# Optimization experiments

Hardware: AMD Instinct MI355X
Metric: run time of the kernel (lower is better)

The kernel has to match this reference:

```python
import jax, jax.numpy as jnp
import numpy as np

V, E, H = 2048, 256, 256
B, T, MMAX = 256, 16, 96  # blocks, max tokens/instr, max instrs/block


def setup_inputs() -> dict:
    key = jax.random.key(0)
    ks = jax.random.split(key, 13)
    # instruction lengths sorted descending (enforce_sorted=True), 96 down to 33
    instr_lens = (96 - (np.arange(B) * 64) // B).astype(np.int64)
    boundaries = np.concatenate([[0], np.cumsum(instr_lens)]).astype(np.int64)
    N = int(boundaries[-1])  # total instructions = 16512
    padded_tokens = jax.random.randint(ks[0], (N, T), 1, V)
    token_lengths = jax.random.randint(ks[1], (N,), 1, T + 1)
    tmask = jnp.arange(T)[None, :] < token_lengths[:, None]
    padded_tokens = jnp.where(tmask, padded_tokens, 0)  # pad with padding_idx=0
    s = 1.0 / np.sqrt(H)
    def u(k, shape):
        return jax.random.uniform(k, shape, jnp.float32, -s, s)
    emb = u(ks[2], (V, E)).at[0].set(0.0)  # padding_idx row is zero
    return dict(
        padded_tokens=padded_tokens.astype(jnp.int64),
        token_lengths=token_lengths.astype(jnp.int64),
        instruction_lengths=jnp.asarray(instr_lens),
        instr_boundaries=jnp.asarray(boundaries),
        embedding=emb,
        w_ih_tok=u(ks[3], (4 * H, E)), w_hh_tok=u(ks[4], (4 * H, H)),
        b_ih_tok=u(ks[5], (4 * H,)), b_hh_tok=u(ks[6], (4 * H,)),
        w_ih_ins=u(ks[7], (4 * H, H)), w_hh_ins=u(ks[8], (4 * H, H)),
        b_ih_ins=u(ks[9], (4 * H,)), b_hh_ins=u(ks[10], (4 * H,)),
        w_lin=u(ks[11], (1, H)), b_lin=u(ks[12], (1,)),
    )


def _lstm_final(x, lengths, w_ih, w_hh, b_ih, b_hh):
    # x: [N, S, D] padded; returns hidden state at last valid step per sequence [N, H]
    N, S, _ = x.shape
    Hh = w_hh.shape[1]
    mask = jnp.arange(S)[:, None] < lengths[None, :]  # [S, N]
    bias = b_ih + b_hh

    def step(carry, inp):
        h, c = carry
        x_t, m = inp  # x_t: [N, D], m: [N]
        g = x_t @ w_ih.T + h @ w_hh.T + bias  # [N, 4H], PyTorch gate order i,f,g,o
        i, f, gg, o = jnp.split(g, 4, axis=-1)
        c_new = jax.nn.sigmoid(f) * c + jax.nn.sigmoid(i) * jnp.tanh(gg)
        h_new = jax.nn.sigmoid(o) * jnp.tanh(c_new)
        m = m[:, None]
        return (jnp.where(m, h_new, h), jnp.where(m, c_new, c)), None

    h0 = jnp.zeros((N, Hh), x.dtype)
    (h, _), _ = jax.lax.scan(step, (h0, h0), (jnp.swapaxes(x, 0, 1), mask))
    return h


def reference(padded_tokens, token_lengths, instruction_lengths, instr_boundaries,
              embedding, w_ih_tok, w_hh_tok, b_ih_tok, b_hh_tok,
              w_ih_ins, w_hh_ins, b_ih_ins, b_hh_ins, w_lin, b_lin):
    # token-level LSTM over all instructions (packed == masked scan)
    emb_tokens = embedding[padded_tokens]  # [N, T, E]
    instr_inputs = _lstm_final(emb_tokens, token_lengths,
                               w_ih_tok, w_hh_tok, b_ih_tok, b_hh_tok)  # [N, H]
    N = instr_inputs.shape[0]
    # regroup instructions into blocks via boundaries (pad_sequence equivalent)
    idx = instr_boundaries[:-1, None] + jnp.arange(MMAX)[None, :]  # [B, MMAX]
    valid = jnp.arange(MMAX)[None, :] < instruction_lengths[:, None]
    gathered = jnp.where(valid[..., None],
                         instr_inputs[jnp.clip(idx, 0, N - 1)], 0.0)  # [B, MMAX, H]
    final = _lstm_final(gathered, instruction_lengths,
                        w_ih_ins, w_hh_ins, b_ih_ins, b_hh_ins)  # [B, H]
    return (final @ w_lin.T + b_lin).squeeze(-1)  # [B]
```

## Files before the change

kernel.cpp:

```cpp
#include <hip/hip_runtime.h>
#include <hip/hip_bf16.h>
#include <math.h>

#define VSZ 2048
#define EDIM 256
#define HDIM 256
#define G4 1024
#define TMAX 16
#define IB 16

typedef _Float16 f16x2 __attribute__((ext_vector_type(2)));
typedef _Float16 f16x4 __attribute__((ext_vector_type(4)));
typedef _Float16 f16x8 __attribute__((ext_vector_type(8)));
typedef float f32x4 __attribute__((ext_vector_type(4)));

#define HA_STRIDE 264
#define GW_STRIDE 260

__device__ __forceinline__ float fexp2(float x) {
#if defined(__has_builtin) && __has_builtin(__builtin_amdgcn_exp2f)
  return __builtin_amdgcn_exp2f(x);
#else
  return exp2f(x);
#endif
}
__device__ __forceinline__ float frcp(float x) {
#if defined(__has_builtin) && __has_builtin(__builtin_amdgcn_rcpf)
  return __builtin_amdgcn_rcpf(x);
#else
  return 1.0f / x;
#endif
}
__device__ __forceinline__ float sigm(float x) {
  return frcp(1.0f + fexp2(x * -1.44269504f));
}
__device__ __forceinline__ float tanh_fast(float x) {
  float t = fexp2(fminf(x, 15.0f) * 2.88539008f);
  return (t - 1.0f) * frcp(t + 1.0f);
}

__device__ __forceinline__ float fdot2(f16x2 a, f16x2 b, float c) {
#if defined(__has_builtin) && __has_builtin(__builtin_amdgcn_fdot2)
  return __builtin_amdgcn_fdot2(a, b, c, false);
#else
  return c + (float)a.x * (float)b.x + (float)a.y * (float)b.y;
#endif
}

__device__ __forceinline__ float dot8h(uint4 w, float4 hv, float acc) {
  f16x2 h0 = __builtin_bit_cast(f16x2, hv.x);
  f16x2 h1 = __builtin_bit_cast(f16x2, hv.y);
  f16x2 h2 = __builtin_bit_cast(f16x2, hv.z);
  f16x2 h3 = __builtin_bit_cast(f16x2, hv.w);
  f16x2 w0 = __builtin_bit_cast(f16x2, w.x);
  f16x2 w1 = __builtin_bit_cast(f16x2, w.y);
  f16x2 w2 = __builtin_bit_cast(f16x2, w.z);
  f16x2 w3 = __builtin_bit_cast(f16x2, w.w);
  return fdot2(h3, w3, fdot2(h2, w2, fdot2(h1, w1, fdot2(h0, w0, acc))));
}

__device__ __forceinline__ bool is_f32(const void* w) {
  const unsigned short* p = (const unsigned short*)w;
  int pl = 0;
#pragma unroll
  for (int i = 0; i < 64; ++i) {
    unsigned e = (p[2 * i] >> 7) & 0xFF;
    pl += (e >= 113 && e <= 122) ? 1 : 0;
  }
  return pl < 48;
}

template <bool F32>
__device__ __forceinline__ float ldf(const void* p, long j) {
  if (F32) return ((const float*)p)[j];
  return __uint_as_float(((unsigned)((const unsigned short*)p)[j]) << 16);
}
__device__ __forceinline__ float ldf_rt(const void* p, long j, bool f32) {
  if (f32) return ((const float*)p)[j];
  return __uint_as_float(((unsigned)((const unsigned short*)p)[j]) << 16);
}
template <bool I64>
__device__ __forceinline__ int ldi(const int* p, int j) {
  return I64 ? p[2 * j] : p[j];
}
__device__ __forceinline__ int ldi_rt(const int* p, int j, bool i64) {
  return i64 ? p[2 * j] : p[j];
}

__global__ __launch_bounds__(256) void k_transp(const void* src, float* __restrict__ dst,
                                                const void* fprobe) {
  __shared__ float tile[32][33];
  __shared__ int sf;
  if (threadIdx.x == 0) sf = is_f32(fprobe) ? 1 : 0;
  __syncthreads();
  const bool f32 = (sf != 0);
  const int tx = threadIdx.x & 31, ty = threadIdx.x >> 5;
  const int r0 = blockIdx.x * 32, c0 = blockIdx.y * 32;
#pragma unroll
  for (int q = 0; q < 4; ++q) {
    int rr = ty + q * 8;
    tile[rr][tx] = ldf_rt(src, (long)(r0 + rr) * 256 + (c0 + tx), f32);
  }
  __syncthreads();
#pragma unroll
  for (int q = 0; q < 4; ++q) {
    int cc = ty + q * 8;
    dst[(size_t)(c0 + cc) * 1024 + (r0 + tx)] = tile[tx][cc];
  }
}

__global__ __launch_bounds__(256) void k_pack(const void* src, uint4* __restrict__ dst,
                                              const void* fprobe) {
  __shared__ int sf;
  if (threadIdx.x == 0) sf = is_f32(fprobe) ? 1 : 0;
  __syncthreads();
  const bool f32 = (sf != 0);
  const int idx = blockIdx.x * 256 + threadIdx.x;
  const int rr = idx & 255, j = (idx >> 8) & 3, c = idx >> 10;
  const long base = (long)(j * 256 + rr) * 256 + 8 * c;
  unsigned u[4];
#pragma unroll
  for (int q = 0; q < 4; ++q) {
    f16x2 v;
    v.x = (_Float16)ldf_rt(src, base + 2 * q, f32);
    v.y = (_Float16)ldf_rt(src, base + 2 * q + 1, f32);
    u[q] = __builtin_bit_cast(unsigned, v);
  }
  uint4 o; o.x = u[0]; o.y = u[1]; o.z = u[2]; o.w = u[3];
  dst[idx] = o;
}

__global__ __launch_bounds__(256) void k_packB(const void* src, f16x8* __restrict__ dst,
                                               const void* fprobe) {
  __shared__ int sf;
  if (threadIdx.x == 0) sf = is_f32(fprobe) ? 1 : 0;
  __syncthreads();
  const bool f32 = (sf != 0);
  const int idx = blockIdx.x * 256 + threadIdx.x;
  const int l = idx & 63;
  int rest = idx >> 6;
  const int kt = rest & 7; rest >>= 3;
  const int nt = rest & 15;
  const int w = rest >> 4;
  const int n = 256 * w + nt * 16 + (l & 15);
  const int j = n & 3, e = n >> 2;
  const long base = (long)(j * 256 + e) * 256 + kt * 32 + ((l >> 4) << 3);
  f16x8 v;
#pragma unroll
  for (int q = 0; q < 8; ++q) v[q] = (_Float16)ldf_rt(src, base + q, f32);
  dst[idx] = v;
}

template <bool F32>
__device__ void tok_table_impl(const void* emb, const float* __restrict__ wT,
                               const void* bih, const void* bhh,
                               f16x4* __restrict__ tabi4, float (*xs)[256]) {
  const int t = threadIdx.x;
  const int v0 = blockIdx.x * 16;
#pragma unroll
  for (int i = 0; i < 16; ++i) xs[i][t] = ldf<F32>(emb, (long)(v0 + i) * EDIM + t);
  __syncthreads();
  float acc[4][16];
#pragma unroll
  for (int j = 0; j < 4; ++j)
#pragma unroll
    for (int i = 0; i < 16; ++i) acc[j][i] = 0.f;
  for (int k4 = 0; k4 < 64; ++k4) {
    float w[4][4];
#pragma unroll
    for (int kk = 0; kk < 4; ++kk)
#pragma unroll
      for (int j = 0; j < 4; ++j)
        w[j][kk] = wT[(size_t)(k4 * 4 + kk) * 1024 + j * 256 + t];
#pragma unroll
    for (int i = 0; i < 16; ++i) {
      float4 h4 = *(const float4*)&xs[i][k4 * 4];
#pragma unroll
      for (int j = 0; j < 4; ++j)
        acc[j][i] = fmaf(h4.x, w[j][0], fmaf(h4.y, w[j][1],
                    fmaf(h4.z, w[j][2], fmaf(h4.w, w[j][3], acc[j][i]))));
    }
  }
  float b[4];
#pragma unroll
  for (int j = 0; j < 4; ++j)
    b[j] = ldf<F32>(bih, j * 256 + t) + ldf<F32>(bhh, j * 256 + t);
#pragma unroll
  for (int i = 0; i < 16; ++i) {
    f16x4 v;
    v.x = (_Float16)(acc[0][i] + b[0]);
    v.y = (_Float16)(acc[1][i] + b[1]);
    v.z = (_Float16)(acc[2][i] + b[2]);
    v.w = (_Float16)(acc[3][i] + b[3]);
    tabi4[(size_t)(v0 + i) * 256 + t] = v;
  }
}

__global__ __launch_bounds__(256) void k_tok_table(
    const void* emb, const float* __restrict__ wT, const void* bih,
    const void* bhh, f16x4* __restrict__ tabi4, const void* fprobe) {
  __shared__ float xs[16][256];
  __shared__ int sf;
  if (threadIdx.x == 0) sf = is_f32(fprobe) ? 1 : 0;
  __syncthreads();
  if (sf) tok_table_impl<true>(emb, wT, bih, bhh, tabi4, xs);
  else    tok_table_impl<false>(emb, wT, bih, bhh, tabi4, xs);
}

__global__ __launch_bounds__(1024) void k_bucket(const int* tlen, int N,
                                                 int* __restrict__ perm,
                                                 const int* iprobe) {
  __shared__ int cnt[16][18];
  __shared__ int wbase[16][18];
  __shared__ int base[18];
  const int t = threadIdx.x;
  const int w = t >> 6;
  const bool i64 = (iprobe[1] == 0);
  if (t < 16 * 18) ((int*)cnt)[t] = 0;
  __syncthreads();
  for (int n = t; n < N; n += 1024) {
    int len = ldi_rt(tlen, n, i64);
    len = max(0, min(16, len));
    atomicAdd(&cnt[w][len], 1);
  }
  __syncthreads();
  if (t < 17) {
    int s = 0;
    for (int ww = 0; ww < 16; ++ww) { wbase[ww][t] = s; s += cnt[ww][t]; }
    base[t] = s;
  }
  __syncthreads();
  if (t == 0) {
    int s = 0;
    for (int i = 0; i <= 16; ++i) { int c = base[i]; base[i] = s; s += c; }
  }
  __syncthreads();
  if (t < 16 * 18) ((int*)cnt)[t] = 0;
  __syncthreads();
  for (int n = t; n < N; n += 1024) {
    int len = ldi_rt(tlen, n, i64);
    len = max(0, min(16, len));
    int pos = base[len] + wbase[w][len] + atomicAdd(&cnt[w][len], 1);
    perm[pos] = n;
  }
}

struct TokSmemM {
  float gateW[4][16 * GW_STRIDE];
  _Float16 hA[16 * HA_STRIDE];
  int tokL[IB][TMAX];
  int lenL[IB];
  int nIdx[IB];
};

template <bool I64>
__device__ void tok_mfma_impl(const int* tok32, const int* tlen32,
                              const int* __restrict__ perm,
                              const f16x4* __restrict__ tabi4,
                              const f16x8* __restrict__ pkB,
                              const f16x8* __restrict__ pkBI,
                              const void* bihI, const void* bhhI,
                              float* __restrict__ instrH, float* __restrict__ gx,
                              int N, int do_gx, bool f32, TokSmemM& sm) {
  const int n0 = blockIdx.x * IB, t = threadIdx.x;
  const int w = t >> 6, l = t & 63;
  if (t < IB) {
    int slot = n0 + t;
    int n = (slot < N) ? perm[slot] : -1;
    sm.nIdx[t] = n;
    sm.lenL[t] = (n >= 0) ? ldi<I64>(tlen32, n) : 0;
  }
  for (int idx = t; idx < 16 * HA_STRIDE / 2; idx += 256) ((unsigned*)sm.hA)[idx] = 0;
  __syncthreads();
  {
    int i = t >> 4, s = t & 15;
    int n = sm.nIdx[i];
    sm.tokL[i][s] = (n >= 0) ? ldi<I64>(tok32, n * TMAX + s) : 0;
  }
  float c[IB];
#pragma unroll
  for (int i = 0; i < IB; ++i) c[i] = 0.f;
  __syncthreads();
  int maxlen = 0;
#pragma unroll
  for (int i = 0; i < IB; ++i) maxlen = max(maxlen, sm.lenL[i]);

  const f16x8* Bp = pkB + (size_t)w * (16 * 8 * 64);
  const int aOff = (l & 15) * HA_STRIDE + ((l >> 4) << 3);
  const int m0 = (l >> 4) << 2;
  float* gw = sm.gateW[w];

  for (int s = 0; s < maxlen; ++s) {
    f16x8 aF[8];
#pragma unroll
    for (int kt = 0; kt < 8; ++kt)
      aF[kt] = *(const f16x8*)&sm.hA[aOff + kt * 32];
#pragma unroll 2
    for (int g4 = 0; g4 < 4; ++g4) {
      f32x4 a0 = {0.f, 0.f, 0.f, 0.f}, a1 = a0, a2 = a0, a3 = a0;
#pragma unroll
      for (int kt = 0; kt < 8; ++kt) {
        const f16x8* bb = Bp + ((size_t)(g4 * 4) * 8 + kt) * 64 + l;
        f16x8 b0 = bb[0 * 8 * 64];
        f16x8 b1 = bb[1 * 8 * 64];
        f16x8 b2 = bb[2 * 8 * 64];
        f16x8 b3 = bb[3 * 8 * 64];
        a0 = __builtin_amdgcn_mfma_f32_16x16x32_f16(aF[kt], b0, a0, 0, 0, 0);
        a1 = __builtin_amdgcn_mfma_f32_16x16x32_f16(aF[kt], b1, a1, 0, 0, 0);
        a2 = __builtin_amdgcn_mfma_f32_16x16x32_f16(aF[kt], b2, a2, 0, 0, 0);
        a3 = __builtin_amdgcn_mfma_f32_16x16x32_f16(aF[kt], b3, a3, 0, 0, 0);
      }
      const int colb = (l & 15);
#pragma unroll
      for (int r = 0; r < 4; ++r) {
        gw[(m0 + r) * GW_STRIDE + (g4 * 4 + 0) * 16 + colb] = a0[r];
        gw[(m0 + r) * GW_STRIDE + (g4 * 4 + 1) * 16 + colb] = a1[r];
        gw[(m0 + r) * GW_STRIDE + (g4 * 4 + 2) * 16 + colb] = a2[r];
        gw[(m0 + r) * GW_STRIDE + (g4 * 4 + 3) * 16 + colb] = a3[r];
      }
    }
    __syncthreads();
#pragma unroll
    for (int m = 0; m < IB; ++m) {
      if (s < sm.lenL[m]) {
        float4 gv = *(const float4*)&gw[m * GW_STRIDE + 4 * l];
        f16x4 tb = tabi4[(size_t)sm.tokL[m][s] * 256 + t];
        float gi = gv.x + (float)tb.x;
        float gf = gv.y + (float)tb.y;
        float gg = gv.z + (float)tb.z;
        float go = gv.w + (float)tb.w;
        float si = sigm(gi), sf = sigm(gf), tg = tanh_fast(gg), so = sigm(go);
        c[m] = sf * c[m] + si * tg;
        sm.hA[m * HA_STRIDE + t] = (_Float16)(so * tanh_fast(c[m]));
      }
    }
    __syncthreads();
  }
#pragma unroll
  for (int m = 0; m < IB; ++m) {
    int n = sm.nIdx[m];
    if (n >= 0) instrH[(size_t)n * HDIM + t] = (float)sm.hA[m * HA_STRIDE + t];
  }
  if (do_gx) {
    f16x8 aF[8];
#pragma unroll
    for (int kt = 0; kt < 8; ++kt)
      aF[kt] = *(const f16x8*)&sm.hA[aOff + kt * 32];
    const f16x8* BpI = pkBI + (size_t)w * (16 * 8 * 64);
#pragma unroll 2
    for (int g4 = 0; g4 < 4; ++g4) {
      f32x4 a0 = {0.f, 0.f, 0.f, 0.f}, a1 = a0, a2 = a0, a3 = a0;
#pragma unroll
      for (int kt = 0; kt < 8; ++kt) {
        const f16x8* bb = BpI + ((size_t)(g4 * 4) * 8 + kt) * 64 + l;
        f16x8 b0 = bb[0 * 8 * 64];
        f16x8 b1 = bb[1 * 8 * 64];
        f16x8 b2 = bb[2 * 8 * 64];
        f16x8 b3 = bb[3 * 8 * 64];
        a0 = __builtin_amdgcn_mfma_f32_16x16x32_f16(aF[kt], b0, a0, 0, 0, 0);
        a1 = __builtin_amdgcn_mfma_f32_16x16x32_f16(aF[kt], b1, a1, 0, 0, 0);
        a2 = __builtin_amdgcn_mfma_f32_16x16x32_f16(aF[kt], b2, a2, 0, 0, 0);
        a3 = __builtin_amdgcn_mfma_f32_16x16x32_f16(aF[kt], b3, a3, 0, 0, 0);
      }
      const int colb = (l & 15);
#pragma unroll
      for (int r = 0; r < 4; ++r) {
        gw[(m0 + r) * GW_STRIDE + (g4 * 4 + 0) * 16 + colb] = a0[r];
        gw[(m0 + r) * GW_STRIDE + (g4 * 4 + 1) * 16 + colb] = a1[r];
        gw[(m0 + r) * GW_STRIDE + (g4 * 4 + 2) * 16 + colb] = a2[r];
        gw[(m0 + r) * GW_STRIDE + (g4 * 4 + 3) * 16 + colb] = a3[r];
      }
    }
    __syncthreads();
    const float bj0 = ldf_rt(bihI, 0 * 256 + t, f32) + ldf_rt(bhhI, 0 * 256 + t, f32);
    const float bj1 = ldf_rt(bihI, 1 * 256 + t, f32) + ldf_rt(bhhI, 1 * 256 + t, f32);
    const float bj2 = ldf_rt(bihI, 2 * 256 + t, f32) + ldf_rt(bhhI, 2 * 256 + t, f32);
    const float bj3 = ldf_rt(bihI, 3 * 256 + t, f32) + ldf_rt(bhhI, 3 * 256 + t, f32);
#pragma unroll
    for (int m = 0; m < IB; ++m) {
      int n = sm.nIdx[m];
      if (n >= 0) {
        float4 gv = *(const float4*)&gw[m * GW_STRIDE + 4 * l];
        gx[(size_t)n * G4 +       t] = gv.x + bj0;
        gx[(size_t)n * G4 + 256 + t] = gv.y + bj1;
        gx[(size_t)n * G4 + 512 + t] = gv.z + bj2;
        gx[(size_t)n * G4 + 768 + t] = gv.w + bj3;
      }
    }
  }
}

__global__ __launch_bounds__(256, 2) void k_tok_lstm(
    const int* tok32, const int* tlen32, const int* __restrict__ perm,
    const f16x4* __restrict__ tabi4, const f16x8* __restrict__ pkB,
    const f16x8* __restrict__ pkBI, const void* bihI, const void* bhhI,
    float* __restrict__ instrH, float* __restrict__ gx, int N, int do_gx,
    const int* iprobe, const void* fprobe) {
  __shared__ TokSmemM sm;
  __shared__ int sfl;
  if (threadIdx.x == 0)
    sfl = ((iprobe[1] == 0) ? 1 : 0) | (is_f32(fprobe) ? 2 : 0);
  __syncthreads();
  const bool f32 = (sfl & 2) != 0;
  if (sfl & 1) tok_mfma_impl<true >(tok32, tlen32, perm, tabi4, pkB, pkBI, bihI, bhhI, instrH, gx, N, do_gx, f32, sm);
  else         tok_mfma_impl<false>(tok32, tlen32, perm, tabi4, pkB, pkBI, bihI, bhhI, instrH, gx, N, do_gx, f32, sm);
}

#define RCH 24
#define LCH 8
struct InsSmem {
  uint4 wL[LCH][1024];
  float gL[1024];
  f16x2 hL2[128];
  float red[256];
};

template <bool F32, bool I64>
__device__ void ins_rec_impl(const int* ilen32, const int* bnd32,
                             const float* __restrict__ gx,
                             const uint4* __restrict__ pk,
                             const void* wlin, const void* blin,
                             float* __restrict__ out, int B, InsSmem& sm) {
  const int b = blockIdx.x, t = threadIdx.x;
  const int j = t >> 8, rr = t & 255;
  const int len = ldi<I64>(ilen32, b);
  const long n0 = (long)ldi<I64>(bnd32, b);
#pragma unroll
  for (int cc = 0; cc < LCH; ++cc)
    sm.wL[cc][t] = pk[((RCH + cc) * 4 + j) * 256 + rr];
  uint4 wr[RCH];
#pragma unroll
  for (int cg = 0; cg < RCH; ++cg)
    wr[cg] = pk[(cg * 4 + j) * 256 + rr];
  if (t < 128) {
    f16x2 z; z.x = (_Float16)0.f; z.y = (_Float16)0.f;
    sm.hL2[t] = z;
  }
  float c = 0.f, h = 0.f;
  __syncthreads();

  for (int m = 0; m < len; ++m) {
    float g0 = 0.f, g1 = 0.f, g2 = 0.f, g3 = 0.f;
    if (t < 256) {
      const float* gp = gx + (size_t)(n0 + m) * G4;
      g0 = gp[t]; g1 = gp[256 + t]; g2 = gp[512 + t]; g3 = gp[768 + t];
    }
    float a0 = 0.f, a1 = 0.f;
#pragma unroll
    for (int cg = 0; cg < RCH; ++cg) {
      float4 hv = ((const float4*)sm.hL2)[cg];
      if (cg & 1) a1 = dot8h(wr[cg], hv, a1);
      else        a0 = dot8h(wr[cg], hv, a0);
    }
#pragma unroll
    for (int cc = 0; cc < LCH; ++cc) {
      float4 hv = ((const float4*)sm.hL2)[RCH + cc];
      if (cc & 1) a1 = dot8h(sm.wL[cc][t], hv, a1);
      else        a0 = dot8h(sm.wL[cc][t], hv, a0);
    }
    sm.gL[t] = a0 + a1;
    __syncthreads();
    if (t < 256) {
      float gi = g0 + sm.gL[t];
      float gf = g1 + sm.gL[256 + t];
      float gg = g2 + sm.gL[512 + t];
      float go = g3 + sm.gL[768 + t];
      float si = sigm(gi), sf = sigm(gf), tg = tanh_fast(gg), so = sigm(go);
      c = sf * c + si * tg;
      h = so * tanh_fast(c);
      ((_Float16*)sm.hL2)[t] = (_Float16)h;
    }
    __syncthreads();
  }
  if (t < 256) sm.red[t] = h * ldf<F32>(wlin, t);
  __syncthreads();
  for (int st = 128; st > 0; st >>= 1) {
    if (t < st) sm.red[t] += sm.red[t + st];
    __syncthreads();
  }
  if (t == 0) out[b] = sm.red[0] + ldf<F32>(blin, 0);
}

__global__ __launch_bounds__(1024) void k_ins_rec(
    const int* ilen32, const int* bnd32, const float* __restrict__ gx,
    const uint4* __restrict__ pk, const void* wlin, const void* blin,
    float* __restrict__ out, int B, const void* fprobe, const int* iprobe) {
  __shared__ InsSmem sm;
  __shared__ int sfl;
  if (threadIdx.x == 0)
    sfl = (is_f32(fprobe) ? 1 : 0) | ((iprobe[1] == 0) ? 2 : 0);
  __syncthreads();
  const int fl = sfl;
  if (fl == 0)      ins_rec_impl<false, false>(ilen32, bnd32, gx, pk, wlin, blin, out, B, sm);
  else if (fl == 1) ins_rec_impl<true,  false>(ilen32, bnd32, gx, pk, wlin, blin, out, B, sm);
  else if (fl == 2) ins_rec_impl<false, true >(ilen32, bnd32, gx, pk, wlin, blin, out, B, sm);
  else              ins_rec_impl<true,  true >(ilen32, bnd32, gx, pk, wlin, blin, out, B, sm);
}

#define IBB 4
struct InsSmemFB {
  float hL[IBB][HDIM];
  float xL[IBB][HDIM];
  float gL[IBB][G4];
};

template <bool F32, bool I64>
__device__ void ins_fb_impl(const int* ilen32, const int* bnd32,
                            const float* __restrict__ instrH,
                            const float* __restrict__ wTih,
                            const float* __restrict__ wThh,
                            const void* bih, const void* bhh,
                            const void* wlin, const void* blin,
                            float* __restrict__ out, int B, InsSmemFB& sm) {
  const int wg = blockIdx.x, t = threadIdx.x;
  const int myblk = t >> 8, myelem = t & 255;
  int len[IBB], n0[IBB];
#pragma unroll
  for (int i = 0; i < IBB; ++i) {
    int b = wg * IBB + i;
    len[i] = (b < B) ? ldi<I64>(ilen32, b) : 0;
    n0[i]  = (b < B) ? ldi<I64>(bnd32, b) : 0;
  }
  float c = 0.f;
  sm.hL[myblk][myelem] = 0.f;
  float bias_r = ldf<F32>(bih, t) + ldf<F32>(bhh, t);
  __syncthreads();
  int maxlen = 0;
#pragma unroll
  for (int i = 0; i < IBB; ++i) maxlen = max(maxlen, len[i]);
  for (int m = 0; m < maxlen; ++m) {
    unsigned act = 0;
#pragma unroll
    for (int i = 0; i < IBB; ++i) if (m < len[i]) act |= (1u << i);
    if (m < len[myblk])
      sm.xL[myblk][myelem] = instrH[(size_t)(n0[myblk] + m) * HDIM + myelem];
    __syncthreads();
    float a[IBB];
#pragma unroll
    for (int i = 0; i < IBB; ++i) a[i] = (act & (1u << i)) ? bias_r : 0.f;
    for (int k4 = 0; k4 < 64; ++k4) {
      float w0 = wThh[(size_t)(k4 * 4 + 0) * 1024 + t];
      float w1 = wThh[(size_t)(k4 * 4 + 1) * 1024 + t];
      float w2 = wThh[(size_t)(k4 * 4 + 2) * 1024 + t];
      float w3 = wThh[(size_t)(k4 * 4 + 3) * 1024 + t];
      float u0 = wTih[(size_t)(k4 * 4 + 0) * 1024 + t];
      float u1 = wTih[(size_t)(k4 * 4 + 1) * 1024 + t];
      float u2 = wTih[(size_t)(k4 * 4 + 2) * 1024 + t];
      float u3 = wTih[(size_t)(k4 * 4 + 3) * 1024 + t];
#pragma unroll
      for (int i = 0; i < IBB; ++i) {
        if (!(act & (1u << i))) continue;
        float4 h4 = *(const float4*)&sm.hL[i][k4 * 4];
        float4 x4 = *(const float4*)&sm.xL[i][k4 * 4];
        a[i] = fmaf(h4.x, w0, fmaf(h4.y, w1, fmaf(h4.z, w2, fmaf(h4.w, w3, a[i]))));
        a[i] = fmaf(x4.x, u0, fmaf(x4.y, u1, fmaf(x4.z, u2, fmaf(x4.w, u3, a[i]))));
      }
    }
#pragma unroll
    for (int i = 0; i < IBB; ++i)
      if (act & (1u << i)) sm.gL[i][t] = a[i];
    __syncthreads();
    if (m < len[myblk]) {
      float si = sigm(sm.gL[myblk][myelem]);
      float sf = sigm(sm.gL[myblk][256 + myelem]);
      float tg = tanh_fast(sm.gL[myblk][512 + myelem]);
      float so = sigm(sm.gL[myblk][768 + myelem]);
      c = sf * c + si * tg;
      sm.hL[myblk][myelem] = so * tanh_fast(c);
    }
    __syncthreads();
  }
  sm.gL[myblk][myelem] = sm.hL[myblk][myelem] * ldf<F32>(wlin, myelem);
  __syncthreads();
  for (int st = 128; st > 0; st >>= 1) {
    if (myelem < st) sm.gL[myblk][myelem] += sm.gL[myblk][myelem + st];
    __syncthreads();
  }
  if (myelem == 0 && wg * IBB + myblk < B)
    out[wg * IBB + myblk] = sm.gL[myblk][0] + ldf<F32>(blin, 0);
}

__global__ __launch_bounds__(1024) void k_ins_fb(
    const int* ilen32, const int* bnd32, const float* __restrict__ instrH,
    const float* __restrict__ wTih, const float* __restrict__ wThh,
    const void* bih, const void* bhh, const void* wlin, const void* blin,
    float* __restrict__ out, int B, const void* fprobe, const int* iprobe) {
  __shared__ InsSmemFB sm;
  __shared__ int sfl;
  if (threadIdx.x == 0)
    sfl = (is_f32(fprobe) ? 1 : 0) | ((iprobe[1] == 0) ? 2 : 0);
  __syncthreads();
  const int fl = sfl;
  if (fl == 0)      ins_fb_impl<false, false>(ilen32, bnd32, instrH, wTih, wThh, bih, bhh, wlin, blin, out, B, sm);
  else if (fl == 1) ins_fb_impl<true,  false>(ilen32, bnd32, instrH, wTih, wThh, bih, bhh, wlin, blin, out, B, sm);
  else if (fl == 2) ins_fb_impl<false, true >(ilen32, bnd32, instrH, wTih, wThh, bih, bhh, wlin, blin, out, B, sm);
  else              ins_fb_impl<true,  true >(ilen32, bnd32, instrH, wTih, wThh, bih, bhh, wlin, blin, out, B, sm);
}

extern "C" void kernel_launch(void* const* d_in, const int* in_sizes, int n_in,
                              void* d_out, int out_size, void* d_ws, size_t ws_size,
                              hipStream_t stream) {
  const int N = in_sizes[1];
  const int B = in_sizes[2];

  float* ws = (float*)d_ws;
  size_t off = 0;
  f16x4* tabi4 = (f16x4*)(ws + off); off += (size_t)VSZ * G4 / 2;
  float* instrH   = ws + off; off += (size_t)N * HDIM;
  float* wT_ihI   = ws + off; off += 262144;
  float* wT_hhI   = ws + off; off += 262144;
  float* wT_ihT   = ws + off; off += 262144;
  f16x8* pkB_tok  = (f16x8*)(ws + off); off += 131072;
  f16x8* pkB_ins  = (f16x8*)(ws + off); off += 131072;
  uint4* pk_ins   = (uint4*)(ws + off); off += 131072;
  int*   permI    = (int*)(ws + off);
  off += ((size_t)N + 15) & ~(size_t)15;
  float* gx       = ws + off;
  const size_t need_gx = (off + (size_t)N * G4) * sizeof(float);
  const bool has_gx = (ws_size >= need_gx);

  const void* fprobe = d_in[5];
  const int*  iprobe = (const int*)d_in[1];

  hipLaunchKernelGGL(k_transp, dim3(32, 8), dim3(256), 0, stream, d_in[5], wT_ihT, fprobe);
  hipLaunchKernelGGL(k_transp, dim3(32, 8), dim3(256), 0, stream, d_in[9], wT_ihI, fprobe);
  hipLaunchKernelGGL(k_transp, dim3(32, 8), dim3(256), 0, stream, d_in[10], wT_hhI, fprobe);
  hipLaunchKernelGGL(k_packB, dim3(128), dim3(256), 0, stream, d_in[6], pkB_tok, fprobe);
  hipLaunchKernelGGL(k_packB, dim3(128), dim3(256), 0, stream, d_in[9], pkB_ins, fprobe);
  hipLaunchKernelGGL(k_pack, dim3(128), dim3(256), 0, stream, d_in[10], pk_ins, fprobe);

  hipLaunchKernelGGL(k_tok_table, dim3(VSZ / 16), dim3(256), 0, stream,
                     d_in[4], wT_ihT, d_in[7], d_in[8], tabi4, fprobe);
  hipLaunchKernelGGL(k_bucket, dim3(1), dim3(1024), 0, stream,
                     (const int*)d_in[1], N, permI, iprobe);
  hipLaunchKernelGGL(k_tok_lstm, dim3((N + IB - 1) / IB), dim3(256), 0, stream,
                     (const int*)d_in[0], (const int*)d_in[1], permI, tabi4,
                     pkB_tok, pkB_ins, d_in[11], d_in[12], instrH, gx, N,
                     has_gx ? 1 : 0, iprobe, fprobe);
  if (has_gx) {
    hipLaunchKernelGGL(k_ins_rec, dim3(B), dim3(1024), 0, stream,
                       (const int*)d_in[2], (const int*)d_in[3], gx, pk_ins,
                       d_in[13], d_in[14], (float*)d_out, B, fprobe, iprobe);
  } else {
    hipLaunchKernelGGL(k_ins_fb, dim3((B + IBB - 1) / IBB), dim3(1024), 0, stream,
                       (const int*)d_in[2], (const int*)d_in[3], instrH,
                       wT_ihI, wT_hhI, d_in[11], d_in[12], d_in[13], d_in[14],
                       (float*)d_out, B, fprobe, iprobe);
  }
}
```

Before: 769.0 us.

## Apply LSTM gate nonlinearity per wave right after MFMA, shrinking gate scratch

The token LSTM step no longer writes all gate pre-activations to a large shared buffer and synchronises the block before the elementwise update. Each wave now applies the cell update for its own 16x16 output tile immediately after each g4 MFMA group, using a small per-wave scratch. This removes one block-wide barrier per step's compute phase and cuts LDS use, which may allow better occupancy. In exchange the per-thread cell state mapping changes, each thread does 16 elementwise updates in a different pattern, a barrier is added before the hA writes, and the loops are fully unrolled, which raises register pressure.

```diff
diff --git a/kernel.cpp b/kernel.cpp
--- a/kernel.cpp
+++ b/kernel.cpp
@@ -15,7 +15,7 @@
 typedef float f32x4 __attribute__((ext_vector_type(4)));
 
 #define HA_STRIDE 264
-#define GW_STRIDE 260
+#define GQ_STRIDE 68
 
 __device__ __forceinline__ float fexp2(float x) {
 #if defined(__has_builtin) && __has_builtin(__builtin_amdgcn_exp2f)
@@ -246,7 +246,7 @@
 }
 
 struct TokSmemM {
-  float gateW[4][16 * GW_STRIDE];
+  float gw4[4][16 * GQ_STRIDE];
   _Float16 hA[16 * HA_STRIDE];
   int tokL[IB][TMAX];
   int lenL[IB];
@@ -288,14 +288,16 @@
   const f16x8* Bp = pkB + (size_t)w * (16 * 8 * 64);
   const int aOff = (l & 15) * HA_STRIDE + ((l >> 4) << 3);
   const int m0 = (l >> 4) << 2;
-  float* gw = sm.gateW[w];
+  const int colb = l & 15;
+  float* gwq = sm.gw4[w];
 
   for (int s = 0; s < maxlen; ++s) {
     f16x8 aF[8];
 #pragma unroll
     for (int kt = 0; kt < 8; ++kt)
       aF[kt] = *(const f16x8*)&sm.hA[aOff + kt * 32];
-#pragma unroll 2
+    __syncthreads();
+#pragma unroll
     for (int g4 = 0; g4 < 4; ++g4) {
       f32x4 a0 = {0.f, 0.f, 0.f, 0.f}, a1 = a0, a2 = a0, a3 = a0;
 #pragma unroll
@@ -310,28 +312,28 @@
         a2 = __builtin_amdgcn_mfma_f32_16x16x32_f16(aF[kt], b2, a2, 0, 0, 0);
         a3 = __builtin_amdgcn_mfma_f32_16x16x32_f16(aF[kt], b3, a3, 0, 0, 0);
       }
-      const int colb = (l & 15);
 #pragma unroll
       for (int r = 0; r < 4; ++r) {
-        gw[(m0 + r) * GW_STRIDE + (g4 * 4 + 0) * 16 + colb] = a0[r];
-        gw[(m0 + r) * GW_STRIDE + (g4 * 4 + 1) * 16 + colb] = a1[r];
-        gw[(m0 + r) * GW_STRIDE + (g4 * 4 + 2) * 16 + colb] = a2[r];
-        gw[(m0 + r) * GW_STRIDE + (g4 * 4 + 3) * 16 + colb] = a3[r];
+        gwq[(m0 + r) * GQ_STRIDE + 0 * 16 + colb] = a0[r];
+        gwq[(m0 + r) * GQ_STRIDE + 1 * 16 + colb] = a1[r];
+        gwq[(m0 + r) * GQ_STRIDE + 2 * 16 + colb] = a2[r];
+        gwq[(m0 + r) * GQ_STRIDE + 3 * 16 + colb] = a3[r];
       }
-    }
-    __syncthreads();
-#pragma unroll
-    for (int m = 0; m < IB; ++m) {
-      if (s < sm.lenL[m]) {
-        float4 gv = *(const float4*)&gw[m * GW_STRIDE + 4 * l];
-        f16x4 tb = tabi4[(size_t)sm.tokL[m][s] * 256 + t];
-        float gi = gv.x + (float)tb.x;
-        float gf = gv.y + (float)tb.y;
-        float gg = gv.z + (float)tb.z;
-        float go = gv.w + (float)tb.w;
-        float si = sigm(gi), sf = sigm(gf), tg = tanh_fast(gg), so = sigm(go);
-        c[m] = sf * c[m] + si * tg;
-        sm.hA[m * HA_STRIDE + t] = (_Float16)(so * tanh_fast(c[m]));
+      const int eg = 64 * w + 16 * g4 + colb;
+#pragma unroll
+      for (int r = 0; r < 4; ++r) {
+        const int m = m0 + r;
+        if (s < sm.lenL[m]) {
+          float4 gv = *(const float4*)&gwq[m * GQ_STRIDE + 4 * colb];
+          f16x4 tb = tabi4[(size_t)sm.tokL[m][s] * 256 + eg];
+          float gi = gv.x + (float)tb.x;
+          float gf = gv.y + (float)tb.y;
+          float gg = gv.z + (float)tb.z;
+          float go = gv.w + (float)tb.w;
+          float si = sigm(gi), sf = sigm(gf), tg = tanh_fast(gg), so = sigm(go);
+          c[g4 * 4 + r] = sf * c[g4 * 4 + r] + si * tg;
+          sm.hA[m * HA_STRIDE + eg] = (_Float16)(so * tanh_fast(c[g4 * 4 + r]));
+        }
       }
     }
     __syncthreads();
@@ -347,7 +349,7 @@
     for (int kt = 0; kt < 8; ++kt)
       aF[kt] = *(const f16x8*)&sm.hA[aOff + kt * 32];
     const f16x8* BpI = pkBI + (size_t)w * (16 * 8 * 64);
-#pragma unroll 2
+#pragma unroll
     for (int g4 = 0; g4 < 4; ++g4) {
       f32x4 a0 = {0.f, 0.f, 0.f, 0.f}, a1 = a0, a2 = a0, a3 = a0;
 #pragma unroll
@@ -362,29 +364,28 @@
         a2 = __builtin_amdgcn_mfma_f32_16x16x32_f16(aF[kt], b2, a2, 0, 0, 0);
         a3 = __builtin_amdgcn_mfma_f32_16x16x32_f16(aF[kt], b3, a3, 0, 0, 0);
       }
-      const int colb = (l & 15);
 #pragma unroll
       for (int r = 0; r < 4; ++r) {
-        gw[(m0 + r) * GW_STRIDE + (g4 * 4 + 0) * 16 + colb] = a0[r];
-        gw[(m0 + r) * GW_STRIDE + (g4 * 4 + 1) * 16 + colb] = a1[r];
-        gw[(m0 + r) * GW_STRIDE + (g4 * 4 + 2) * 16 + colb] = a2[r];
-        gw[(m0 + r) * GW_STRIDE + (g4 * 4 + 3) * 16 + colb] = a3[r];
+        gwq[(m0 + r) * GQ_STRIDE + 0 * 16 + colb] = a0[r];
+        gwq[(m0 + r) * GQ_STRIDE + 1 * 16 + colb] = a1[r];
+        gwq[(m0 + r) * GQ_STRIDE + 2 * 16 + colb] = a2[r];
+        gwq[(m0 + r) * GQ_STRIDE + 3 * 16 + colb] = a3[r];
       }
-    }
-    __syncthreads();
-    const float bj0 = ldf_rt(bihI, 0 * 256 + t, f32) + ldf_rt(bhhI, 0 * 256 + t, f32);
-    const float bj1 = ldf_rt(bihI, 1 * 256 + t, f32) + ldf_rt(bhhI, 1 * 256 + t, f32);
-    const float bj2 = ldf_rt(bihI, 2 * 256 + t, f32) + ldf_rt(bhhI, 2 * 256 + t, f32);
-    const float bj3 = ldf_rt(bihI, 3 * 256 + t, f32) + ldf_rt(bhhI, 3 * 256 + t, f32);
-#pragma unroll
-    for (int m = 0; m < IB; ++m) {
-      int n = sm.nIdx[m];
-      if (n >= 0) {
-        float4 gv = *(const float4*)&gw[m * GW_STRIDE + 4 * l];
-        gx[(size_t)n * G4 +       t] = gv.x + bj0;
-        gx[(size_t)n * G4 + 256 + t] = gv.y + bj1;
-        gx[(size_t)n * G4 + 512 + t] = gv.z + bj2;
-        gx[(size_t)n * G4 + 768 + t] = gv.w + bj3;
+      const int eg = 64 * w + 16 * g4 + colb;
+      float bj0 = ldf_rt(bihI, 0 * 256 + eg, f32) + ldf_rt(bhhI, 0 * 256 + eg, f32);
+      float bj1 = ldf_rt(bihI, 1 * 256 + eg, f32) + ldf_rt(bhhI, 1 * 256 + eg, f32);
+      float bj2 = ldf_rt(bihI, 2 * 256 + eg, f32) + ldf_rt(bhhI, 2 * 256 + eg, f32);
+      float bj3 = ldf_rt(bihI, 3 * 256 + eg, f32) + ldf_rt(bhhI, 3 * 256 + eg, f32);
+#pragma unroll
+      for (int r = 0; r < 4; ++r) {
+        int n = sm.nIdx[m0 + r];
+        if (n >= 0) {
+          float4 gv = *(const float4*)&gwq[(m0 + r) * GQ_STRIDE + 4 * colb];
+          gx[(size_t)n * G4 +       eg] = gv.x + bj0;
+          gx[(size_t)n * G4 + 256 + eg] = gv.y + bj1;
+          gx[(size_t)n * G4 + 512 + eg] = gv.z + bj2;
+          gx[(size_t)n * G4 + 768 + eg] = gv.w + bj3;
+        }
       }
     }
   }
```

Measured after the change: 1.381 ms. +79.6%, slower.
